# Optimization experiments

Measured on AMD Instinct MI355X. Metric: run time of the kernel, lower is better.

## Reference

```python
import jax, jax.numpy as jnp
import numpy as np

M, L = 256, 256
E_EDGES = L - 1
EPS = 1e-12
HX, HZ, JZ = 3.0, 0.25, -1.0


def setup_inputs() -> dict:
    key = jax.random.key(0)
    k1, k2 = jax.random.split(key, 2)
    # original: uniform(-pi/2, pi/2); narrowed to keep cos(theta_m - theta_b) away from 0
    theta = jax.random.uniform(k1, (M, L), minval=-0.3, maxval=0.3, dtype=jnp.float32)
    coef = jax.random.uniform(k2, (M,), minval=-1.0, maxval=1.0, dtype=jnp.float32)
    edges_u = jnp.arange(E_EDGES, dtype=jnp.int32)       # 1D chain
    edges_v = edges_u + 1
    strengths = jnp.ones((E_EDGES,), dtype=jnp.float32)
    return {"theta": theta, "coef": coef, "edges_u": edges_u,
            "edges_v": edges_v, "strengths": strengths}


def reference(theta, coef, edges_u, edges_v, strengths):
    # theta: [M, L], coef: [M]
    cos_m = jnp.cos(theta)
    sin_m = jnp.sin(theta)
    cm = cos_m[:, None, :]   # [M,1,L] -> row m
    sm = sin_m[:, None, :]
    cb = cos_m[None, :, :]   # [1,M,L] -> row b
    sb = sin_m[None, :, :]
    # pairwise angle-sum/difference trig, all [M, M, L]
    cosd = cm * cb + sm * sb            # cos(theta_m - theta_b)
    sind = sm * cb - cm * sb            # sin(theta_m - theta_b)
    sins = sm * cb + cm * sb            # sin(theta_m + theta_b)
    coss = cm * cb - sm * sb            # cos(theta_m + theta_b)
    inv = 1.0 / (cosd + EPS)

    P = jnp.prod(cosd, axis=-1)                     # [M,M] overlap products
    U = jnp.sum(sins * inv, axis=-1)                # [M,M] sigma_x amplitude ratios
    V = jnp.sum(coss * inv, axis=-1)                # [M,M] sigma_z amplitude ratios
    a = coss * inv                                  # [M,M,L] per-site z ratio

    # ZZ interaction over graph edges
    Szz = jnp.einsum('e,mbe->mb', strengths,
                     a[:, :, edges_u] * a[:, :, edges_v])  # [M,M]

    F_total = HZ * V + HX * U + JZ * Szz            # [M,M]
    base = coef[:, None] * coef[None, :] * P        # [M,M]
    N = jnp.sum(base * F_total)
    D = jnp.sum(base)

    cP = coef[None, :] * P                          # c_b * P
    dN_dc = 2.0 * jnp.sum(cP * F_total, axis=1)     # [M]
    dD_dc = 2.0 * jnp.sum(cP, axis=1)               # [M]

    g_d = -sind * inv                               # d log cosd / d theta_mq
    Gxz = (-HZ * sins + HX * coss) * inv + (HZ * coss + HX * sins) * (sind * inv * inv)

    # incident-edge neighbor sums: inc[m,b,q] = sum_{e incident to q} s_e * a[m,b,nbr]
    uu = jnp.concatenate([edges_u, edges_v])
    vv = jnp.concatenate([edges_v, edges_u])
    ss = jnp.concatenate([strengths, strengths])
    inc = jnp.zeros_like(a).at[:, :, uu].add(ss * a[:, :, vv])
    Gzz = (-sins * inv + coss * (sind * inv * inv)) * inc * JZ

    w = base[:, :, None]                            # [M,M,1]
    dD_dtheta = 2.0 * jnp.sum(w * g_d, axis=1)      # [M,L]
    dN_dtheta = 2.0 * jnp.sum(
        w * (g_d * F_total[:, :, None] + Gxz + Gzz), axis=1)  # [M,L]

    E = N / D
    dE_dc = (dN_dc - E * dD_dc) / D
    dE_dtheta = (dN_dtheta - E * dD_dtheta) / D
    return dE_dtheta, dE_dc, E / L
```

## Files before the change

### kernel.cpp

```cpp
#include <hip/hip_runtime.h>
#include <math.h>

#define HXc 3.0f
#define HZc 0.25f
#define JZc (-1.0f)

#define OFF_TANR 0
#define OFF_TANT 65536
#define OFF_CPR  131072
#define OFF_DNT  131328
#define OFF_DDT  262400
#define OFF_NM   393472
#define OFF_DM   393984
#define OFF_CN   394496
#define OFF_CD   395008

__device__ __forceinline__ float tan_poly(float x) {
    float y = x * x;
    float p = fmaf(y, 62.0f / 2835.0f, 17.0f / 315.0f);
    p = fmaf(y, p, 2.0f / 15.0f);
    p = fmaf(y, p, 1.0f / 3.0f);
    return x * fmaf(y, p, 1.0f);
}

__device__ __forceinline__ float cos_poly(float x) {
    float y = x * x;
    float p = fmaf(y, 1.0f / 40320.0f, -1.0f / 720.0f);
    p = fmaf(y, p, 1.0f / 24.0f);
    p = fmaf(y, p, -0.5f);
    return fmaf(y, p, 1.0f);
}

__global__ __launch_bounds__(256) void k_prep(const float* __restrict__ theta,
                                              float* __restrict__ ws) {
    int m = blockIdx.x, t = threadIdx.x;
    float x = theta[m * 256 + t];
    float tn = tan_poly(x);
    float c = cos_poly(x);
    ws[OFF_TANR + m * 256 + t] = tn;
    ws[OFF_TANT + t * 256 + m] = tn;
    float pr = c;
    for (int o = 32; o; o >>= 1) pr *= __shfl_xor(pr, o);
    __shared__ float pp[4];
    if ((t & 63) == 0) pp[t >> 6] = pr;
    __syncthreads();
    if (t == 0) ws[OFF_CPR + m] = pp[0] * pp[1] * pp[2] * pp[3];
}

__global__ __launch_bounds__(512) void k_main(
        const float* __restrict__ coef,
        const float* __restrict__ strengths,
        float* __restrict__ ws) {
    int g = blockIdx.x;
    int m = g >> 1;
    int boff = (g & 1) * 128;
    int tid = threadIdx.x;
    const float* __restrict__ tanR = ws + OFF_TANR;
    const float* __restrict__ tanT = ws + OFF_TANT;
    const float* __restrict__ Cpr = ws + OFF_CPR;

    __shared__ float sLDS[256];
    __shared__ float tmL[256];
    __shared__ float4 quart[4][128];
    __shared__ float Flds[128], cPlds[128];
    __shared__ float wr[2][4];
    __shared__ float gN[8 * 256];
    __shared__ float gD[8 * 256];

    if (tid < 256) {
        sLDS[tid] = (tid < 255) ? strengths[tid] : 0.0f;
        tmL[tid] = tanR[m * 256 + tid];
    }
    __syncthreads();

    {
        int bl = tid & 127, q = tid >> 7;
        int b = boff + bl;
        int l0 = q * 64;
        float pw = 1.0f, u = 0.0f, v = 0.0f, z = 0.0f, a_prev = 0.0f;
        if (q) {
            int l = l0 - 1;
            float qq = tmL[l] * tanT[l * 256 + b];
            a_prev = (1.0f - qq) * __builtin_amdgcn_rcpf(1.0f + qq);
        }
        for (int l = l0; l < l0 + 64; ++l) {
            float tm = tmL[l];
            float tb = tanT[l * 256 + b];
            float qq = tm * tb;
            float w1 = 1.0f + qq;
            float inv = __builtin_amdgcn_rcpf(w1);
            pw *= w1;
            u = fmaf(tm + tb, inv, u);
            float a = (1.0f - qq) * inv;
            v += a;
            float sPrev = (l > 0) ? sLDS[l - 1] : 0.0f;
            z = fmaf(sPrev * a_prev, a, z);
            a_prev = a;
        }
        quart[q][bl] = make_float4(pw, u, v, z);
    }
    __syncthreads();

    if (tid < 128) {
        int b = boff + tid;
        float4 A = quart[0][tid], B = quart[1][tid];
        float4 C = quart[2][tid], Dq = quart[3][tid];
        float P = Cpr[m] * Cpr[b] * (A.x * B.x * C.x * Dq.x);
        float U = A.y + B.y + C.y + Dq.y;
        float V = A.z + B.z + C.z + Dq.z;
        float Z = A.w + B.w + C.w + Dq.w;
        float F = HZc * V + HXc * U + JZc * Z;
        float cP = coef[b] * P;
        Flds[tid] = F;
        cPlds[tid] = cP;
        float base = coef[m] * cP;
        float s1 = base, s2 = base * F, s3 = cP, s4 = cP * F;
        for (int o = 32; o; o >>= 1) {
            s1 += __shfl_xor(s1, o);
            s2 += __shfl_xor(s2, o);
            s3 += __shfl_xor(s3, o);
            s4 += __shfl_xor(s4, o);
        }
        if ((tid & 63) == 0) {
            int w = tid >> 6;
            wr[w][0] = s1; wr[w][1] = s2; wr[w][2] = s3; wr[w][3] = s4;
        }
    }
    __syncthreads();
    if (tid == 0) {
        ws[OFF_DM + g] = wr[0][0] + wr[1][0];
        ws[OFF_NM + g] = wr[0][1] + wr[1][1];
        ws[OFF_CD + g] = wr[0][2] + wr[1][2];
        ws[OFF_CN + g] = wr[0][3] + wr[1][3];
    }

    {
        int w = tid >> 6, lane = tid & 63;
        int l0 = lane * 4;
        float coefm = coef[m];
        float4 tm4 = *(const float4*)&tmL[l0];
        float tm[4] = {tm4.x, tm4.y, tm4.z, tm4.w};
        float sR[4], sL[4];
#pragma unroll
        for (int j = 0; j < 4; ++j) {
            int l = l0 + j;
            sR[j] = sLDS[l];
            sL[j] = (l > 0) ? sLDS[l - 1] : 0.0f;
        }
        float pN[4] = {0.f, 0.f, 0.f, 0.f};
        float pD[4] = {0.f, 0.f, 0.f, 0.f};

        for (int i = 0; i < 16; ++i) {
            int bl = w * 16 + i;
            int b = boff + bl;
            float4 tb4 = *(const float4*)&tanR[b * 256 + l0];
            float tb[4] = {tb4.x, tb4.y, tb4.z, tb4.w};
            float Fv = Flds[bl];
            float base = coefm * cPlds[bl];

            float A[4], S[4], G[4];
#pragma unroll
            for (int j = 0; j < 4; ++j) {
                float qq = tm[j] * tb[j];
                float w1 = 1.0f + qq;
                float inv = __builtin_amdgcn_rcpf(w1);
                A[j] = (1.0f - qq) * inv;
                S[j] = (tm[j] + tb[j]) * inv;
                G[j] = (tm[j] - tb[j]) * inv;
            }
            float aLn = __shfl_up(A[3], 1);
            if (lane == 0) aLn = 0.0f;
            float aRn = __shfl_down(A[0], 1);
            if (lane == 63) aRn = 0.0f;
            float am1[4] = {aLn, A[0], A[1], A[2]};
            float ap1[4] = {A[1], A[2], A[3], aRn};
#pragma unroll
            for (int j = 0; j < 4; ++j) {
                float Gxz = fmaf(HXc, A[j], -HZc * S[j])
                          + fmaf(HZc, A[j], HXc * S[j]) * G[j];
                float K = JZc * fmaf(A[j], G[j], -S[j]);
                float inc = fmaf(sR[j], ap1[j], sL[j] * am1[j]);
                float term = fmaf(Fv, -G[j], fmaf(K, inc, Gxz));
                pN[j] = fmaf(base, term, pN[j]);
                pD[j] = fmaf(base, -G[j], pD[j]);
            }
        }
        ((float4*)gN)[w * 64 + lane] = make_float4(pN[0], pN[1], pN[2], pN[3]);
        ((float4*)gD)[w * 64 + lane] = make_float4(pD[0], pD[1], pD[2], pD[3]);
    }
    __syncthreads();
    if (tid < 256) {
        float sn = 0.0f, sd = 0.0f;
#pragma unroll
        for (int ww = 0; ww < 8; ++ww) {
            sn += gN[ww * 256 + tid];
            sd += gD[ww * 256 + tid];
        }
        ws[OFF_DNT + g * 256 + tid] = sn;
        ws[OFF_DDT + g * 256 + tid] = sd;
    }
}

__global__ __launch_bounds__(256) void k_fin(const float* __restrict__ ws,
                                             float* __restrict__ out) {
    int m = blockIdx.x, t = threadIdx.x;
    float nv = ws[OFF_NM + t] + ws[OFF_NM + 256 + t];
    float dv = ws[OFF_DM + t] + ws[OFF_DM + 256 + t];
    for (int o = 32; o; o >>= 1) {
        nv += __shfl_xor(nv, o);
        dv += __shfl_xor(dv, o);
    }
    __shared__ float rn[4], rd[4];
    if ((t & 63) == 0) { rn[t >> 6] = nv; rd[t >> 6] = dv; }
    __syncthreads();
    float N = rn[0] + rn[1] + rn[2] + rn[3];
    float D = rd[0] + rd[1] + rd[2] + rd[3];
    float E = N / D;
    float invD = 1.0f / D;
    int g0 = m * 2, g1 = m * 2 + 1;
    float sn = ws[OFF_DNT + g0 * 256 + t] + ws[OFF_DNT + g1 * 256 + t];
    float sd = ws[OFF_DDT + g0 * 256 + t] + ws[OFF_DDT + g1 * 256 + t];
    out[m * 256 + t] = 2.0f * invD * (sn - E * sd);
    if (t == 0) {
        float cn = ws[OFF_CN + g0] + ws[OFF_CN + g1];
        float cd = ws[OFF_CD + g0] + ws[OFF_CD + g1];
        out[65536 + m] = 2.0f * invD * (cn - E * cd);
    }
    if (m == 0 && t == 1) out[65792] = E * (1.0f / 256.0f);
}

extern "C" void kernel_launch(void* const* d_in, const int* in_sizes, int n_in,
                              void* d_out, int out_size, void* d_ws, size_t ws_size,
                              hipStream_t stream) {
    const float* theta = (const float*)d_in[0];
    const float* coef = (const float*)d_in[1];
    const float* strengths = (const float*)d_in[4];
    float* out = (float*)d_out;
    float* ws = (float*)d_ws;

    k_prep<<<256, 256, 0, stream>>>(theta, ws);
    k_main<<<512, 512, 0, stream>>>(coef, strengths, ws);
    k_fin<<<256, 256, 0, stream>>>(ws, out);
}
```

Measured before the change: 87.43 us.

## Fuse final normalization into main kernel via last-block atomic counter

Removes the separate finalize kernel: each main block bumps an atomic counter after a threadfence, and the last block to finish reduces N and D and writes all outputs with float4 stores. It also rewrites a few inner-loop expressions as fmas, deriving S from G to save a multiply. This saves one kernel launch and its gap, but the whole 256x256 output is then written by a single block, which serialises that tail work.

```diff
diff --git a/kernel.cpp b/kernel.cpp
--- a/kernel.cpp
+++ b/kernel.cpp
@@ -14,6 +14,7 @@
 #define OFF_DM   393984
 #define OFF_CN   394496
 #define OFF_CD   395008
+#define OFF_CNT  395520
 
 __device__ __forceinline__ float tan_poly(float x) {
     float y = x * x;
@@ -45,12 +46,14 @@
     if ((t & 63) == 0) pp[t >> 6] = pr;
     __syncthreads();
     if (t == 0) ws[OFF_CPR + m] = pp[0] * pp[1] * pp[2] * pp[3];
+    if (m == 0 && t == 0) ((unsigned*)(ws + OFF_CNT))[0] = 0u;
 }
 
 __global__ __launch_bounds__(512) void k_main(
         const float* __restrict__ coef,
         const float* __restrict__ strengths,
-        float* __restrict__ ws) {
+        float* __restrict__ ws,
+        float* __restrict__ out) {
     int g = blockIdx.x;
     int m = g >> 1;
     int boff = (g & 1) * 128;
@@ -91,7 +94,7 @@
             float inv = __builtin_amdgcn_rcpf(w1);
             pw *= w1;
             u = fmaf(tm + tb, inv, u);
-            float a = (1.0f - qq) * inv;
+            float a = fmaf(-qq, inv, inv);
             v += a;
             float sPrev = (l > 0) ? sLDS[l - 1] : 0.0f;
             z = fmaf(sPrev * a_prev, a, z);
@@ -140,6 +143,7 @@
         float coefm = coef[m];
         float4 tm4 = *(const float4*)&tmL[l0];
         float tm[4] = {tm4.x, tm4.y, tm4.z, tm4.w};
+        float tm2[4] = {2.0f * tm4.x, 2.0f * tm4.y, 2.0f * tm4.z, 2.0f * tm4.w};
         float sR[4], sL[4];
 #pragma unroll
         for (int j = 0; j < 4; ++j) {
@@ -164,9 +168,9 @@
                 float qq = tm[j] * tb[j];
                 float w1 = 1.0f + qq;
                 float inv = __builtin_amdgcn_rcpf(w1);
-                A[j] = (1.0f - qq) * inv;
-                S[j] = (tm[j] + tb[j]) * inv;
                 G[j] = (tm[j] - tb[j]) * inv;
+                S[j] = fmaf(tm2[j], inv, -G[j]);
+                A[j] = fmaf(-qq, inv, inv);
             }
             float aLn = __shfl_up(A[3], 1);
             if (lane == 0) aLn = 0.0f;
@@ -178,11 +182,12 @@
             for (int j = 0; j < 4; ++j) {
                 float Gxz = fmaf(HXc, A[j], -HZc * S[j])
                           + fmaf(HZc, A[j], HXc * S[j]) * G[j];
-                float K = JZc * fmaf(A[j], G[j], -S[j]);
+                float K = fmaf(-A[j], G[j], S[j]);
                 float inc = fmaf(sR[j], ap1[j], sL[j] * am1[j]);
-                float term = fmaf(Fv, -G[j], fmaf(K, inc, Gxz));
+                float term = fmaf(K, inc, Gxz);
+                term = fmaf(-Fv, G[j], term);
                 pN[j] = fmaf(base, term, pN[j]);
-                pD[j] = fmaf(base, -G[j], pD[j]);
+                pD[j] = fmaf(-base, G[j], pD[j]);
             }
         }
         ((float4*)gN)[w * 64 + lane] = make_float4(pN[0], pN[1], pN[2], pN[3]);
@@ -199,34 +204,59 @@
         ws[OFF_DNT + g * 256 + tid] = sn;
         ws[OFF_DDT + g * 256 + tid] = sd;
     }
-}
-
-__global__ __launch_bounds__(256) void k_fin(const float* __restrict__ ws,
-                                             float* __restrict__ out) {
-    int m = blockIdx.x, t = threadIdx.x;
-    float nv = ws[OFF_NM + t] + ws[OFF_NM + 256 + t];
-    float dv = ws[OFF_DM + t] + ws[OFF_DM + 256 + t];
+
+    __threadfence();
+    __shared__ unsigned lastFlag;
+    if (tid == 0) {
+        unsigned prev = atomicAdd((unsigned*)(ws + OFF_CNT), 1u);
+        lastFlag = (prev == 511u) ? 1u : 0u;
+    }
+    __syncthreads();
+    if (!lastFlag) return;
+    __threadfence();
+
+    float nv = ws[OFF_NM + tid], dv = ws[OFF_DM + tid];
     for (int o = 32; o; o >>= 1) {
         nv += __shfl_xor(nv, o);
         dv += __shfl_xor(dv, o);
     }
-    __shared__ float rn[4], rd[4];
-    if ((t & 63) == 0) { rn[t >> 6] = nv; rd[t >> 6] = dv; }
-    __syncthreads();
-    float N = rn[0] + rn[1] + rn[2] + rn[3];
-    float D = rd[0] + rd[1] + rd[2] + rd[3];
-    float E = N / D;
-    float invD = 1.0f / D;
-    int g0 = m * 2, g1 = m * 2 + 1;
-    float sn = ws[OFF_DNT + g0 * 256 + t] + ws[OFF_DNT + g1 * 256 + t];
-    float sd = ws[OFF_DDT + g0 * 256 + t] + ws[OFF_DDT + g1 * 256 + t];
-    out[m * 256 + t] = 2.0f * invD * (sn - E * sd);
-    if (t == 0) {
-        float cn = ws[OFF_CN + g0] + ws[OFF_CN + g1];
-        float cd = ws[OFF_CD + g0] + ws[OFF_CD + g1];
-        out[65536 + m] = 2.0f * invD * (cn - E * cd);
-    }
-    if (m == 0 && t == 1) out[65792] = E * (1.0f / 256.0f);
+    __shared__ float rn[8], rd[8];
+    if ((tid & 63) == 0) { rn[tid >> 6] = nv; rd[tid >> 6] = dv; }
+    __syncthreads();
+    __shared__ float scal2[2];
+    if (tid == 0) {
+        float N = 0.0f, D = 0.0f;
+#pragma unroll
+        for (int k = 0; k < 8; ++k) { N += rn[k]; D += rd[k]; }
+        scal2[0] = N / D;
+        scal2[1] = 1.0f / D;
+    }
+    __syncthreads();
+    float E = scal2[0], invD = scal2[1];
+    float s2 = 2.0f * invD;
+
+    const float4* dnt4 = (const float4*)(ws + OFF_DNT);
+    const float4* ddt4 = (const float4*)(ws + OFF_DDT);
+    float4* out4 = (float4*)out;
+    for (int i = tid; i < 16384; i += 512) {
+        int mI = i >> 6, l4 = i & 63;
+        float4 a0 = dnt4[(mI * 2) * 64 + l4];
+        float4 a1 = dnt4[(mI * 2 + 1) * 64 + l4];
+        float4 b0 = ddt4[(mI * 2) * 64 + l4];
+        float4 b1 = ddt4[(mI * 2 + 1) * 64 + l4];
+        float4 r;
+        r.x = s2 * ((a0.x + a1.x) - E * (b0.x + b1.x));
+        r.y = s2 * ((a0.y + a1.y) - E * (b0.y + b1.y));
+        r.z = s2 * ((a0.z + a1.z) - E * (b0.z + b1.z));
+        r.w = s2 * ((a0.w + a1.w) - E * (b0.w + b1.w));
+        out4[i] = r;
+    }
+    if (tid < 256) {
+        float cn = ws[OFF_CN + 2 * tid] + ws[OFF_CN + 2 * tid + 1];
+        float cd = ws[OFF_CD + 2 * tid] + ws[OFF_CD + 2 * tid + 1];
+        out[65536 + tid] = s2 * (cn - E * cd);
+    }
+    if (tid == 0) out[65792] = E * (1.0f / 256.0f);
 }
 
 extern "C" void kernel_launch(void* const* d_in, const int* in_sizes, int n_in,
@@ -239,6 +269,5 @@
     float* ws = (float*)d_ws;
 
     k_prep<<<256, 256, 0, stream>>>(theta, ws);
-    k_main<<<512, 512, 0, stream>>>(coef, strengths, ws);
-    k_fin<<<256, 256, 0, stream>>>(ws, out);
-}
+    k_main<<<512, 512, 0, stream>>>(coef, strengths, ws, out);
+}
```

Result: slower. 168.3 us (+92.5%).

## Fuse trig prep into main kernel, recomputing tan/cos on the fly from theta

Applied to the files above, without the earlier changes.

Removes the separate prep kernel that precomputed tan rows, a transposed tan table and per-row cos products into workspace. The main kernel now evaluates tan and cos polynomials directly from theta for both the m row and each b row, folding the per-b cos product into the running product. This saves a kernel launch and the workspace round trip plus the strided transposed reads. In exchange it adds redundant polynomial arithmetic across blocks. The phase-1 loop now reads theta row-wise with float4 loads instead of column-strided, and a few expressions are folded into FMAs.

```diff
diff --git a/kernel.cpp b/kernel.cpp
--- a/kernel.cpp
+++ b/kernel.cpp
@@ -3,17 +3,13 @@
 
 #define HXc 3.0f
 #define HZc 0.25f
-#define JZc (-1.0f)
-
-#define OFF_TANR 0
-#define OFF_TANT 65536
-#define OFF_CPR  131072
-#define OFF_DNT  131328
-#define OFF_DDT  262400
-#define OFF_NM   393472
-#define OFF_DM   393984
-#define OFF_CN   394496
-#define OFF_CD   395008
+
+#define OFF_DNT  0
+#define OFF_DDT  131072
+#define OFF_NM   262144
+#define OFF_DM   262656
+#define OFF_CN   263168
+#define OFF_CD   263680
 
 __device__ __forceinline__ float tan_poly(float x) {
     float y = x * x;
@@ -31,23 +27,8 @@
     return fmaf(y, p, 1.0f);
 }
 
-__global__ __launch_bounds__(256) void k_prep(const float* __restrict__ theta,
-                                              float* __restrict__ ws) {
-    int m = blockIdx.x, t = threadIdx.x;
-    float x = theta[m * 256 + t];
-    float tn = tan_poly(x);
-    float c = cos_poly(x);
-    ws[OFF_TANR + m * 256 + t] = tn;
-    ws[OFF_TANT + t * 256 + m] = tn;
-    float pr = c;
-    for (int o = 32; o; o >>= 1) pr *= __shfl_xor(pr, o);
-    __shared__ float pp[4];
-    if ((t & 63) == 0) pp[t >> 6] = pr;
-    __syncthreads();
-    if (t == 0) ws[OFF_CPR + m] = pp[0] * pp[1] * pp[2] * pp[3];
-}
-
 __global__ __launch_bounds__(512) void k_main(
+        const float* __restrict__ theta,
         const float* __restrict__ coef,
         const float* __restrict__ strengths,
         float* __restrict__ ws) {
@@ -55,12 +36,10 @@
     int m = g >> 1;
     int boff = (g & 1) * 128;
     int tid = threadIdx.x;
-    const float* __restrict__ tanR = ws + OFF_TANR;
-    const float* __restrict__ tanT = ws + OFF_TANT;
-    const float* __restrict__ Cpr = ws + OFF_CPR;
 
     __shared__ float sLDS[256];
     __shared__ float tmL[256];
+    __shared__ float prp[4];
     __shared__ float4 quart[4][128];
     __shared__ float Flds[128], cPlds[128];
     __shared__ float wr[2][4];
@@ -68,34 +47,47 @@
     __shared__ float gD[8 * 256];
 
     if (tid < 256) {
+        float x = theta[m * 256 + tid];
         sLDS[tid] = (tid < 255) ? strengths[tid] : 0.0f;
-        tmL[tid] = tanR[m * 256 + tid];
-    }
-    __syncthreads();
+        tmL[tid] = tan_poly(x);
+        float pr = cos_poly(x);
+        for (int o = 32; o; o >>= 1) pr *= __shfl_xor(pr, o);
+        if ((tid & 63) == 0) prp[tid >> 6] = pr;
+    }
+    __syncthreads();
+    float Cpm = prp[0] * prp[1] * prp[2] * prp[3];
 
     {
         int bl = tid & 127, q = tid >> 7;
         int b = boff + bl;
+        const float* __restrict__ thb = theta + b * 256;
         int l0 = q * 64;
         float pw = 1.0f, u = 0.0f, v = 0.0f, z = 0.0f, a_prev = 0.0f;
         if (q) {
-            int l = l0 - 1;
-            float qq = tmL[l] * tanT[l * 256 + b];
+            float tb = tan_poly(thb[l0 - 1]);
+            float qq = tmL[l0 - 1] * tb;
             a_prev = (1.0f - qq) * __builtin_amdgcn_rcpf(1.0f + qq);
         }
-        for (int l = l0; l < l0 + 64; ++l) {
-            float tm = tmL[l];
-            float tb = tanT[l * 256 + b];
-            float qq = tm * tb;
-            float w1 = 1.0f + qq;
-            float inv = __builtin_amdgcn_rcpf(w1);
-            pw *= w1;
-            u = fmaf(tm + tb, inv, u);
-            float a = (1.0f - qq) * inv;
-            v += a;
-            float sPrev = (l > 0) ? sLDS[l - 1] : 0.0f;
-            z = fmaf(sPrev * a_prev, a, z);
-            a_prev = a;
+        for (int l4 = l0; l4 < l0 + 64; l4 += 4) {
+            float4 th4 = *(const float4*)&thb[l4];
+            float th[4] = {th4.x, th4.y, th4.z, th4.w};
+#pragma unroll
+            for (int j = 0; j < 4; ++j) {
+                int l = l4 + j;
+                float tb = tan_poly(th[j]);
+                float cb = cos_poly(th[j]);
+                float tm = tmL[l];
+                float qq = tm * tb;
+                float w1 = 1.0f + qq;
+                float inv = __builtin_amdgcn_rcpf(w1);
+                pw *= cb * w1;
+                u = fmaf(tm + tb, inv, u);
+                float a = fmaf(-qq, inv, inv);
+                v += a;
+                float sPrev = (l > 0) ? sLDS[l - 1] : 0.0f;
+                z = fmaf(sPrev * a_prev, a, z);
+                a_prev = a;
+            }
         }
         quart[q][bl] = make_float4(pw, u, v, z);
     }
@@ -105,11 +97,11 @@
         int b = boff + tid;
         float4 A = quart[0][tid], B = quart[1][tid];
         float4 C = quart[2][tid], Dq = quart[3][tid];
-        float P = Cpr[m] * Cpr[b] * (A.x * B.x * C.x * Dq.x);
+        float P = Cpm * (A.x * B.x * C.x * Dq.x);
         float U = A.y + B.y + C.y + Dq.y;
         float V = A.z + B.z + C.z + Dq.z;
         float Z = A.w + B.w + C.w + Dq.w;
-        float F = HZc * V + HXc * U + JZc * Z;
+        float F = HZc * V + HXc * U - Z;
         float cP = coef[b] * P;
         Flds[tid] = F;
         cPlds[tid] = cP;
@@ -140,6 +132,7 @@
         float coefm = coef[m];
         float4 tm4 = *(const float4*)&tmL[l0];
         float tm[4] = {tm4.x, tm4.y, tm4.z, tm4.w};
+        float tm2[4] = {2.0f * tm4.x, 2.0f * tm4.y, 2.0f * tm4.z, 2.0f * tm4.w};
         float sR[4], sL[4];
 #pragma unroll
         for (int j = 0; j < 4; ++j) {
@@ -153,8 +146,9 @@
         for (int i = 0; i < 16; ++i) {
             int bl = w * 16 + i;
             int b = boff + bl;
-            float4 tb4 = *(const float4*)&tanR[b * 256 + l0];
-            float tb[4] = {tb4.x, tb4.y, tb4.z, tb4.w};
+            float4 th4 = *(const float4*)&theta[b * 256 + l0];
+            float tb[4] = {tan_poly(th4.x), tan_poly(th4.y),
+                           tan_poly(th4.z), tan_poly(th4.w)};
             float Fv = Flds[bl];
             float base = coefm * cPlds[bl];
 
@@ -164,9 +158,9 @@
                 float qq = tm[j] * tb[j];
                 float w1 = 1.0f + qq;
                 float inv = __builtin_amdgcn_rcpf(w1);
-                A[j] = (1.0f - qq) * inv;
-                S[j] = (tm[j] + tb[j]) * inv;
                 G[j] = (tm[j] - tb[j]) * inv;
+                S[j] = fmaf(tm2[j], inv, -G[j]);
+                A[j] = fmaf(-qq, inv, inv);
             }
             float aLn = __shfl_up(A[3], 1);
             if (lane == 0) aLn = 0.0f;
@@ -178,11 +172,12 @@
             for (int j = 0; j < 4; ++j) {
                 float Gxz = fmaf(HXc, A[j], -HZc * S[j])
                           + fmaf(HZc, A[j], HXc * S[j]) * G[j];
-                float K = JZc * fmaf(A[j], G[j], -S[j]);
+                float K = fmaf(-A[j], G[j], S[j]);
                 float inc = fmaf(sR[j], ap1[j], sL[j] * am1[j]);
-                float term = fmaf(Fv, -G[j], fmaf(K, inc, Gxz));
+                float term = fmaf(K, inc, Gxz);
+                term = fmaf(-Fv, G[j], term);
                 pN[j] = fmaf(base, term, pN[j]);
-                pD[j] = fmaf(base, -G[j], pD[j]);
+                pD[j] = fmaf(-base, G[j], pD[j]);
             }
         }
         ((float4*)gN)[w * 64 + lane] = make_float4(pN[0], pN[1], pN[2], pN[3]);
@@ -238,7 +233,6 @@
     float* out = (float*)d_out;
     float* ws = (float*)d_ws;
 
-    k_prep<<<256, 256, 0, stream>>>(theta, ws);
-    k_main<<<512, 512, 0, stream>>>(coef, strengths, ws);
+    k_main<<<512, 512, 0, stream>>>(theta, coef, strengths, ws);
     k_fin<<<256, 256, 0, stream>>>(ws, out);
 }
```

After: 94.12 us. 7.6% more time.

## Split into forward and gradient kernels, folding E into gradient accumulation

Applied to the files above, without the earlier changes.

The main kernel is split into a forward pass that writes per-pair F and cP to workspace, and a gradient kernel that first reduces N and D to get E. The gradient kernel folds E into a shifted F, so only one accumulator is needed and the separate dD/dtheta sum and the finalize kernel go away. A few trig-ratio computations are also rewritten as fmas. The cost is an extra global round trip for F and cP, and the gradient grid shrinks to 256 blocks, each looping over all 256 b values.

```diff
diff --git a/kernel.cpp b/kernel.cpp
--- a/kernel.cpp
+++ b/kernel.cpp
@@ -3,17 +3,16 @@
 
 #define HXc 3.0f
 #define HZc 0.25f
-#define JZc (-1.0f)
 
 #define OFF_TANR 0
 #define OFF_TANT 65536
 #define OFF_CPR  131072
-#define OFF_DNT  131328
-#define OFF_DDT  262400
-#define OFF_NM   393472
-#define OFF_DM   393984
-#define OFF_CN   394496
-#define OFF_CD   395008
+#define OFF_F    131328
+#define OFF_CP   196864
+#define OFF_NM   262400
+#define OFF_DM   262912
+#define OFF_CN   263424
+#define OFF_CD   263936
 
 __device__ __forceinline__ float tan_poly(float x) {
     float y = x * x;
@@ -47,7 +46,7 @@
     if (t == 0) ws[OFF_CPR + m] = pp[0] * pp[1] * pp[2] * pp[3];
 }
 
-__global__ __launch_bounds__(512) void k_main(
+__global__ __launch_bounds__(512) void k_fwd(
         const float* __restrict__ coef,
         const float* __restrict__ strengths,
         float* __restrict__ ws) {
@@ -62,10 +61,7 @@
     __shared__ float sLDS[256];
     __shared__ float tmL[256];
     __shared__ float4 quart[4][128];
-    __shared__ float Flds[128], cPlds[128];
     __shared__ float wr[2][4];
-    __shared__ float gN[8 * 256];
-    __shared__ float gD[8 * 256];
 
     if (tid < 256) {
         sLDS[tid] = (tid < 255) ? strengths[tid] : 0.0f;
@@ -91,7 +87,7 @@
             float inv = __builtin_amdgcn_rcpf(w1);
             pw *= w1;
             u = fmaf(tm + tb, inv, u);
-            float a = (1.0f - qq) * inv;
+            float a = fmaf(-qq, inv, inv);
             v += a;
             float sPrev = (l > 0) ? sLDS[l - 1] : 0.0f;
             z = fmaf(sPrev * a_prev, a, z);
@@ -109,10 +105,10 @@
         float U = A.y + B.y + C.y + Dq.y;
         float V = A.z + B.z + C.z + Dq.z;
         float Z = A.w + B.w + C.w + Dq.w;
-        float F = HZc * V + HXc * U + JZc * Z;
+        float F = fmaf(HZc, V, fmaf(HXc, U, -Z));
         float cP = coef[b] * P;
-        Flds[tid] = F;
-        cPlds[tid] = cP;
+        ws[OFF_F + m * 256 + b] = F;
+        ws[OFF_CP + m * 256 + b] = cP;
         float base = coef[m] * cP;
         float s1 = base, s2 = base * F, s3 = cP, s4 = cP * F;
         for (int o = 32; o; o >>= 1) {
@@ -133,13 +129,45 @@
         ws[OFF_CD + g] = wr[0][2] + wr[1][2];
         ws[OFF_CN + g] = wr[0][3] + wr[1][3];
     }
+}
+
+__global__ __launch_bounds__(512) void k_grad(
+        const float* __restrict__ coef,
+        const float* __restrict__ strengths,
+        const float* __restrict__ ws,
+        float* __restrict__ out) {
+    int m = blockIdx.x, tid = threadIdx.x;
+    const float* __restrict__ tanR = ws + OFF_TANR;
+    __shared__ float sLDS[256], Flds[256], cPlds[256];
+    __shared__ float gN[8 * 256];
+    __shared__ float rn[4], rd[4];
+
+    if (tid < 256) {
+        sLDS[tid] = (tid < 255) ? strengths[tid] : 0.0f;
+        Flds[tid] = ws[OFF_F + m * 256 + tid];
+        cPlds[tid] = ws[OFF_CP + m * 256 + tid];
+        float nv = ws[OFF_NM + tid] + ws[OFF_NM + 256 + tid];
+        float dv = ws[OFF_DM + tid] + ws[OFF_DM + 256 + tid];
+        for (int o = 32; o; o >>= 1) {
+            nv += __shfl_xor(nv, o);
+            dv += __shfl_xor(dv, o);
+        }
+        if ((tid & 63) == 0) { rn[tid >> 6] = nv; rd[tid >> 6] = dv; }
+    }
+    __syncthreads();
+    float N = rn[0] + rn[1] + rn[2] + rn[3];
+    float D = rd[0] + rd[1] + rd[2] + rd[3];
+    float E = N / D;
+    float invD = 1.0f / D;
+    float s2 = 2.0f * invD;
 
     {
         int w = tid >> 6, lane = tid & 63;
         int l0 = lane * 4;
         float coefm = coef[m];
-        float4 tm4 = *(const float4*)&tmL[l0];
+        float4 tm4 = *(const float4*)&tanR[m * 256 + l0];
         float tm[4] = {tm4.x, tm4.y, tm4.z, tm4.w};
+        float tm2[4] = {2.0f * tm4.x, 2.0f * tm4.y, 2.0f * tm4.z, 2.0f * tm4.w};
         float sR[4], sL[4];
 #pragma unroll
         for (int j = 0; j < 4; ++j) {
@@ -148,15 +176,13 @@
             sL[j] = (l > 0) ? sLDS[l - 1] : 0.0f;
         }
         float pN[4] = {0.f, 0.f, 0.f, 0.f};
-        float pD[4] = {0.f, 0.f, 0.f, 0.f};
-
-        for (int i = 0; i < 16; ++i) {
-            int bl = w * 16 + i;
-            int b = boff + bl;
+
+        for (int i = 0; i < 32; ++i) {
+            int b = w * 32 + i;
             float4 tb4 = *(const float4*)&tanR[b * 256 + l0];
             float tb[4] = {tb4.x, tb4.y, tb4.z, tb4.w};
-            float Fv = Flds[bl];
-            float base = coefm * cPlds[bl];
+            float Fp = Flds[b] - E;
+            float base = coefm * cPlds[b];
 
             float A[4], S[4], G[4];
 #pragma unroll
@@ -164,9 +190,9 @@
                 float qq = tm[j] * tb[j];
                 float w1 = 1.0f + qq;
                 float inv = __builtin_amdgcn_rcpf(w1);
-                A[j] = (1.0f - qq) * inv;
-                S[j] = (tm[j] + tb[j]) * inv;
                 G[j] = (tm[j] - tb[j]) * inv;
+                S[j] = fmaf(tm2[j], inv, -G[j]);
+                A[j] = fmaf(-qq, inv, inv);
             }
             float aLn = __shfl_up(A[3], 1);
             if (lane == 0) aLn = 0.0f;
@@ -178,55 +204,29 @@
             for (int j = 0; j < 4; ++j) {
                 float Gxz = fmaf(HXc, A[j], -HZc * S[j])
                           + fmaf(HZc, A[j], HXc * S[j]) * G[j];
-                float K = JZc * fmaf(A[j], G[j], -S[j]);
+                float K = fmaf(-A[j], G[j], S[j]);
                 float inc = fmaf(sR[j], ap1[j], sL[j] * am1[j]);
-                float term = fmaf(Fv, -G[j], fmaf(K, inc, Gxz));
+                float term = fmaf(K, inc, Gxz);
+                term = fmaf(-Fp, G[j], term);
                 pN[j] = fmaf(base, term, pN[j]);
-                pD[j] = fmaf(base, -G[j], pD[j]);
             }
         }
         ((float4*)gN)[w * 64 + lane] = make_float4(pN[0], pN[1], pN[2], pN[3]);
-        ((float4*)gD)[w * 64 + lane] = make_float4(pD[0], pD[1], pD[2], pD[3]);
     }
     __syncthreads();
     if (tid < 256) {
-        float sn = 0.0f, sd = 0.0f;
-#pragma unroll
-        for (int ww = 0; ww < 8; ++ww) {
-            sn += gN[ww * 256 + tid];
-            sd += gD[ww * 256 + tid];
-        }
-        ws[OFF_DNT + g * 256 + tid] = sn;
-        ws[OFF_DDT + g * 256 + tid] = sd;
-    }
-}
-
-__global__ __launch_bounds__(256) void k_fin(const float* __restrict__ ws,
-                                             float* __restrict__ out) {
-    int m = blockIdx.x, t = threadIdx.x;
-    float nv = ws[OFF_NM + t] + ws[OFF_NM + 256 + t];
-    float dv = ws[OFF_DM + t] + ws[OFF_DM + 256 + t];
-    for (int o = 32; o; o >>= 1) {
-        nv += __shfl_xor(nv, o);
-        dv += __shfl_xor(dv, o);
-    }
-    __shared__ float rn[4], rd[4];
-    if ((t & 63) == 0) { rn[t >> 6] = nv; rd[t >> 6] = dv; }
-    __syncthreads();
-    float N = rn[0] + rn[1] + rn[2] + rn[3];
-    float D = rd[0] + rd[1] + rd[2] + rd[3];
-    float E = N / D;
-    float invD = 1.0f / D;
-    int g0 = m * 2, g1 = m * 2 + 1;
-    float sn = ws[OFF_DNT + g0 * 256 + t] + ws[OFF_DNT + g1 * 256 + t];
-    float sd = ws[OFF_DDT + g0 * 256 + t] + ws[OFF_DDT + g1 * 256 + t];
-    out[m * 256 + t] = 2.0f * invD * (sn - E * sd);
-    if (t == 0) {
-        float cn = ws[OFF_CN + g0] + ws[OFF_CN + g1];
-        float cd = ws[OFF_CD + g0] + ws[OFF_CD + g1];
-        out[65536 + m] = 2.0f * invD * (cn - E * cd);
-    }
-    if (m == 0 && t == 1) out[65792] = E * (1.0f / 256.0f);
+        float sn = 0.0f;
+#pragma unroll
+        for (int ww = 0; ww < 8; ++ww) sn += gN[ww * 256 + tid];
+        out[m * 256 + tid] = s2 * sn;
+    }
+    if (tid == 0) {
+        float cn = ws[OFF_CN + 2 * m] + ws[OFF_CN + 2 * m + 1];
+        float cd = ws[OFF_CD + 2 * m] + ws[OFF_CD + 2 * m + 1];
+        out[65536 + m] = s2 * (cn - E * cd);
+    }
+    if (m == 0 && tid == 1)
+        out[65792] = E * (1.0f / 256.0f);
 }
 
 extern "C" void kernel_launch(void* const* d_in, const int* in_sizes, int n_in,
@@ -239,6 +239,6 @@
     float* ws = (float*)d_ws;
 
     k_prep<<<256, 256, 0, stream>>>(theta, ws);
-    k_main<<<512, 512, 0, stream>>>(coef, strengths, ws);
-    k_fin<<<256, 256, 0, stream>>>(ws, out);
-}
+    k_fwd<<<512, 512, 0, stream>>>(coef, strengths, ws);
+    k_grad<<<256, 512, 0, stream>>>(coef, strengths, ws, out);
+}
```

Result: no change. 89.12 us (+1.9%).
